# Performance work log

Measured on AMD Instinct MI355X. Metric: run time of the kernel, lower is better.

The kernel has to match this reference:

```python
import jax, jax.numpy as jnp
import numpy as np

EPS = 1e-7  # tf.keras.backend.epsilon()
ROUTING_ITERS = 3


def setup_inputs() -> dict:
    key = jax.random.key(0)
    k1, k2 = jax.random.split(key)
    B, I, Din = 64, 4096, 8
    N, D = 10, 16
    inputs = jax.random.normal(k1, (B, I, Din), dtype=jnp.float32)
    # glorot_uniform-ish init for W [I, N, Din, D]
    limit = (6.0 / (Din + D)) ** 0.5
    W = jax.random.uniform(k2, (I, N, Din, D), dtype=jnp.float32, minval=-limit, maxval=limit)
    return {"inputs": inputs, "W": W}


def _elementwise_squash(s):
    # Original squashes over axis=-2 of [B,1,N,1,D], a size-1 axis ->
    # the reduce_sum is a no-op and squash becomes elementwise.
    sq = s * s
    scale = sq / (1.0 + sq) / jnp.sqrt(sq + EPS)
    return scale * s


def reference(inputs, W):
    # inputs: [B, I, Din], W: [I, N, Din, D]
    # u_hat[b,i,n,d] = sum_p inputs[b,i,p] * W[i,n,p,d]  (the tile+matmul)
    u_hat = jnp.einsum('bip,inpd->bind', inputs, W)  # [B, I, N, D]
    B, I, N, D = u_hat.shape
    b = jnp.zeros((B, I, N, 1), dtype=u_hat.dtype)
    v = None
    for it in range(ROUTING_ITERS):
        c = jax.nn.softmax(b, axis=2)                 # [B, I, N, 1]
        s = jnp.sum(c * u_hat, axis=1)                # [B, N, D]
        v = _elementwise_squash(s)                    # [B, N, D]
        if it < ROUTING_ITERS - 1:
            # agreement: sum over D -> [B, I, N, 1]
            b = b + jnp.sum(u_hat * v[:, None, :, :], axis=-1, keepdims=True)
    # original: squeeze(v[B,1,N,1,D], axis=1) -> [B, N, 1, D]
    return v[:, :, None, :]
```

## Files before the change

kernel.cpp:

```cpp
#include <hip/hip_runtime.h>
#include <math.h>

#define B_ 64
#define I_ 4096
#define P_ 8
#define N_ 10
#define D_ 16
#define ND_ 160
#define BND_ (B_*ND_)
#define EPS_ 1e-7f

#define IPB_ 8
#define ROWS_ (I_ / IPB_)
#define WTILE_ (N_ * P_ * D_)
#define LGS_ 11

__global__ __launch_bounds__(256)
void xT_kernel(const float* __restrict__ x, float* __restrict__ xT)
{
    int idx = blockIdx.x * 256 + threadIdx.x;
    int p = idx & 7;
    int i = (idx >> 3) & (I_ - 1);
    int b = idx >> 15;
    xT[((size_t)i * B_ + b) * P_ + p] = x[idx];
}

template<int MODE>
__global__ __launch_bounds__(320)
void digitcaps_pass(const float* __restrict__ xT, const float* __restrict__ W,
                    const float* __restrict__ Vc, float* __restrict__ part)
{
    __shared__ float wsh[IPB_ * WTILE_];
    __shared__ float lgsh[(MODE == 1) ? 2 : 1][B_][LGS_];
    const int t = threadIdx.x;
    const int b = t & 63;
    const int w = t >> 6;
    const int n0 = 2 * w;
    const int i0 = blockIdx.x * IPB_;

    {
        const float4* __restrict__ Wg = (const float4*)(W + (size_t)i0 * WTILE_);
        float4* __restrict__ Ws = (float4*)wsh;
#pragma unroll
        for (int c = 0; c < (IPB_ * WTILE_) / 4 / 320; ++c)
            Ws[c * 320 + t] = Wg[c * 320 + t];
    }

    float vc[2][D_];
    if (MODE == 1) {
#pragma unroll
        for (int q = 0; q < 2; ++q) {
            const float4* vp = (const float4*)(Vc + (size_t)b * ND_ + (n0 + q) * D_);
#pragma unroll
            for (int d4 = 0; d4 < 4; ++d4) {
                float4 vv = vp[d4];
                vc[q][d4 * 4 + 0] = vv.x; vc[q][d4 * 4 + 1] = vv.y;
                vc[q][d4 * 4 + 2] = vv.z; vc[q][d4 * 4 + 3] = vv.w;
            }
        }
    }

    float acc[2][D_];
#pragma unroll
    for (int q = 0; q < 2; ++q)
#pragma unroll
        for (int d = 0; d < D_; ++d) acc[q][d] = 0.f;

    float xv[P_];
    {
        const float4* xp = (const float4*)(xT + ((size_t)i0 * B_ + b) * P_);
        float4 a0 = xp[0], a1 = xp[1];
        xv[0]=a0.x; xv[1]=a0.y; xv[2]=a0.z; xv[3]=a0.w;
        xv[4]=a1.x; xv[5]=a1.y; xv[6]=a1.z; xv[7]=a1.w;
    }

    __syncthreads();

#pragma unroll 1
    for (int il = 0; il < IPB_; ++il) {
        const float* __restrict__ Wt = wsh + il * WTILE_ + n0 * (P_ * D_);
        float tv[2][D_];
#pragma unroll
        for (int q = 0; q < 2; ++q) {
            const float* __restrict__ Wq = Wt + q * (P_ * D_);
#pragma unroll
            for (int d = 0; d < D_; ++d) tv[q][d] = 0.f;
#pragma unroll
            for (int p = 0; p < P_; ++p) {
                const float4* __restrict__ wp = (const float4*)(Wq + p * D_);
#pragma unroll
                for (int d4 = 0; d4 < 4; ++d4) {
                    float4 wv = wp[d4];
                    tv[q][d4 * 4 + 0] = fmaf(wv.x, xv[p], tv[q][d4 * 4 + 0]);
                    tv[q][d4 * 4 + 1] = fmaf(wv.y, xv[p], tv[q][d4 * 4 + 1]);
                    tv[q][d4 * 4 + 2] = fmaf(wv.z, xv[p], tv[q][d4 * 4 + 2]);
                    tv[q][d4 * 4 + 3] = fmaf(wv.w, xv[p], tv[q][d4 * 4 + 3]);
                }
            }
        }

        float xn[P_];
        if (il + 1 < IPB_) {
            const float4* xp = (const float4*)(xT + ((size_t)(i0 + il + 1) * B_ + b) * P_);
            float4 a0 = xp[0], a1 = xp[1];
            xn[0]=a0.x; xn[1]=a0.y; xn[2]=a0.z; xn[3]=a0.w;
            xn[4]=a1.x; xn[5]=a1.y; xn[6]=a1.z; xn[7]=a1.w;
        }

        if (MODE == 0) {
#pragma unroll
            for (int q = 0; q < 2; ++q)
#pragma unroll
                for (int d = 0; d < D_; ++d) acc[q][d] += tv[q][d];
        } else {
            float lgq[2];
#pragma unroll
            for (int q = 0; q < 2; ++q) {
                float lA = 0.f, lB = 0.f;
#pragma unroll
                for (int d = 0; d < 8; ++d) {
                    lA = fmaf(tv[q][d], vc[q][d], lA);
                    lB = fmaf(tv[q][d + 8], vc[q][d + 8], lB);
                }
                lgq[q] = lA + lB;
            }
            const int buf = il & 1;
            lgsh[buf][b][n0]     = lgq[0];
            lgsh[buf][b][n0 + 1] = lgq[1];
            __syncthreads();
            float lg[N_];
#pragma unroll
            for (int n = 0; n < N_; ++n) lg[n] = lgsh[buf][b][n];
            float m = lg[0];
#pragma unroll
            for (int n = 1; n < N_; ++n) m = fmaxf(m, lg[n]);
            float se = 0.f;
#pragma unroll
            for (int n = 0; n < N_; ++n) se += __expf(lg[n] - m);
            float inv = 1.f / se;
            float cq0 = __expf(lgq[0] - m) * inv;
            float cq1 = __expf(lgq[1] - m) * inv;
#pragma unroll
            for (int d = 0; d < D_; ++d) {
                acc[0][d] = fmaf(cq0, tv[0][d], acc[0][d]);
                acc[1][d] = fmaf(cq1, tv[1][d], acc[1][d]);
            }
        }

#pragma unroll
        for (int p = 0; p < P_; ++p) xv[p] = xn[p];
    }

    float* __restrict__ po = part + (size_t)blockIdx.x * BND_;
#pragma unroll
    for (int q = 0; q < 2; ++q)
#pragma unroll
        for (int d = 0; d < D_; ++d)
            po[((n0 + q) * D_ + d) * B_ + b] = acc[q][d];
}

__global__ __launch_bounds__(256)
void digitcaps_reduce(const float* __restrict__ part, int rows,
                      float scale, int mode,
                      float* __restrict__ Vc, float* __restrict__ out)
{
    __shared__ float sm[4][16];
    const int t = threadIdx.x;
    const int kk = t & 15;
    const int tp = t >> 4;
    const int k = blockIdx.x * 16 + kk;

    float s = 0.f;
    const int steps = rows >> 4;
    const float* __restrict__ p0 = part + (size_t)tp * BND_ + k;
    const size_t stride = (size_t)16 * BND_;
#pragma unroll 8
    for (int j = 0; j < steps; ++j)
        s += p0[(size_t)j * stride];

    s += __shfl_down(s, 32);
    s += __shfl_down(s, 16);
    if ((t & 63) < 16) sm[t >> 6][kk] = s;
    __syncthreads();

    if (t < 16) {
        float tot = (sm[0][t] + sm[1][t]) + (sm[2][t] + sm[3][t]);
        tot *= scale;
        float sq = tot * tot;
        float v = tot * (sq / ((1.f + sq) * sqrtf(sq + EPS_)));
        int k2 = blockIdx.x * 16 + t;
        int j = (k2 & 63) * ND_ + (k2 >> 6);
        if (mode == 0)      Vc[j] = v;
        else if (mode == 1) Vc[j] += v;
        else                out[j] = v;
    }
}

extern "C" void kernel_launch(void* const* d_in, const int* in_sizes, int n_in,
                              void* d_out, int out_size, void* d_ws, size_t ws_size,
                              hipStream_t stream)
{
    const float* x = (const float*)d_in[0];
    const float* W = (const float*)d_in[1];
    float* out = (float*)d_out;

    float* part = (float*)d_ws;
    float* Vc   = part + (size_t)ROWS_ * BND_;
    float* xT   = Vc + BND_;

    dim3 pblk(320), pgrid(ROWS_), rblk(256), rgrid(BND_ / 16);

    xT_kernel<<<dim3((B_ * I_ * P_) / 256), dim3(256), 0, stream>>>(x, xT);

    for (int pass = 0; pass < 3; ++pass) {
        if (pass == 0)
            digitcaps_pass<0><<<pgrid, pblk, 0, stream>>>(xT, W, nullptr, part);
        else
            digitcaps_pass<1><<<pgrid, pblk, 0, stream>>>(xT, W, Vc, part);
        digitcaps_reduce<<<rgrid, rblk, 0, stream>>>(part, ROWS_,
                                                     pass == 0 ? 0.1f : 1.0f, pass, Vc, out);
    }
}
```

Baseline: 186.9 us.

## Remap threads to 4 lanes per batch with DPP softmax and drop transpose

The pass kernel now gives each batch element 4 lanes (n parity × d half), so each wave covers 16 batches and a block has 256 threads. The softmax over capsules uses DPP lane exchanges instead of a shared-memory logits buffer and __syncthreads on every input row. The separate x transpose kernel is removed; x is read directly in its native layout and partials are written b-major with float4 stores. The trade-off is uncoalesced x reads (each lane group reads different batches), 4x redundant x loads per batch, and more work per thread.

```diff
diff --git a/kernel.cpp b/kernel.cpp
--- a/kernel.cpp
+++ b/kernel.cpp
@@ -11,64 +11,58 @@
 #define EPS_ 1e-7f
 
 #define IPB_ 8
-#define ROWS_ (I_ / IPB_)
+#define NBLK_ (I_ / IPB_)
 #define WTILE_ (N_ * P_ * D_)
-#define LGS_ 11
-
-__global__ __launch_bounds__(256)
-void xT_kernel(const float* __restrict__ x, float* __restrict__ xT)
-{
-    int idx = blockIdx.x * 256 + threadIdx.x;
-    int p = idx & 7;
-    int i = (idx >> 3) & (I_ - 1);
-    int b = idx >> 15;
-    xT[((size_t)i * B_ + b) * P_ + p] = x[idx];
+
+template<int CTRL>
+__device__ __forceinline__ float dpp_bcast(float v) {
+    int r = __builtin_amdgcn_update_dpp(0, __float_as_int(v), CTRL, 0xF, 0xF, true);
+    return __int_as_float(r);
 }
 
 template<int MODE>
-__global__ __launch_bounds__(320)
-void digitcaps_pass(const float* __restrict__ xT, const float* __restrict__ W,
+__global__ __launch_bounds__(256, 2)
+void digitcaps_pass(const float* __restrict__ x, const float* __restrict__ W,
                     const float* __restrict__ Vc, float* __restrict__ part)
 {
     __shared__ float wsh[IPB_ * WTILE_];
-    __shared__ float lgsh[(MODE == 1) ? 2 : 1][B_][LGS_];
     const int t = threadIdx.x;
-    const int b = t & 63;
-    const int w = t >> 6;
-    const int n0 = 2 * w;
+    const int lane = t & 63;
+    const int dh = lane & 1;
+    const int np = (lane >> 1) & 1;
+    const int bl = lane >> 2;
+    const int wv = t >> 6;
+    const int b  = wv * 16 + bl;
     const int i0 = blockIdx.x * IPB_;
 
     {
         const float4* __restrict__ Wg = (const float4*)(W + (size_t)i0 * WTILE_);
         float4* __restrict__ Ws = (float4*)wsh;
 #pragma unroll
-        for (int c = 0; c < (IPB_ * WTILE_) / 4 / 320; ++c)
-            Ws[c * 320 + t] = Wg[c * 320 + t];
-    }
-
-    float vc[2][D_];
+        for (int c = 0; c < (IPB_ * WTILE_) / (4 * 256); ++c)
+            Ws[c * 256 + t] = Wg[c * 256 + t];
+    }
+
+    float vc[5][8];
     if (MODE == 1) {
 #pragma unroll
-        for (int q = 0; q < 2; ++q) {
-            const float4* vp = (const float4*)(Vc + (size_t)b * ND_ + (n0 + q) * D_);
-#pragma unroll
-            for (int d4 = 0; d4 < 4; ++d4) {
-                float4 vv = vp[d4];
-                vc[q][d4 * 4 + 0] = vv.x; vc[q][d4 * 4 + 1] = vv.y;
-                vc[q][d4 * 4 + 2] = vv.z; vc[q][d4 * 4 + 3] = vv.w;
-            }
-        }
-    }
-
-    float acc[2][D_];
-#pragma unroll
-    for (int q = 0; q < 2; ++q)
-#pragma unroll
-        for (int d = 0; d < D_; ++d) acc[q][d] = 0.f;
+        for (int k = 0; k < 5; ++k) {
+            const float4* vp = (const float4*)(Vc + (size_t)b * ND_ + (np + 2 * k) * D_ + dh * 8);
+            float4 v0 = vp[0], v1 = vp[1];
+            vc[k][0]=v0.x; vc[k][1]=v0.y; vc[k][2]=v0.z; vc[k][3]=v0.w;
+            vc[k][4]=v1.x; vc[k][5]=v1.y; vc[k][6]=v1.z; vc[k][7]=v1.w;
+        }
+    }
+
+    float acc[5][8];
+#pragma unroll
+    for (int k = 0; k < 5; ++k)
+#pragma unroll
+        for (int d = 0; d < 8; ++d) acc[k][d] = 0.f;
 
     float xv[P_];
     {
-        const float4* xp = (const float4*)(xT + ((size_t)i0 * B_ + b) * P_);
+        const float4* xp = (const float4*)(x + ((size_t)b * I_ + i0) * P_);
         float4 a0 = xp[0], a1 = xp[1];
         xv[0]=a0.x; xv[1]=a0.y; xv[2]=a0.z; xv[3]=a0.w;
         xv[4]=a1.x; xv[5]=a1.y; xv[6]=a1.z; xv[7]=a1.w;
@@ -78,30 +72,33 @@
 
 #pragma unroll 1
     for (int il = 0; il < IPB_; ++il) {
-        const float* __restrict__ Wt = wsh + il * WTILE_ + n0 * (P_ * D_);
-        float tv[2][D_];
-#pragma unroll
-        for (int q = 0; q < 2; ++q) {
-            const float* __restrict__ Wq = Wt + q * (P_ * D_);
-#pragma unroll
-            for (int d = 0; d < D_; ++d) tv[q][d] = 0.f;
+        const float* __restrict__ Wt = wsh + il * WTILE_ + dh * 8;
+
+        float tv[5][8];
+#pragma unroll
+        for (int k = 0; k < 5; ++k) {
+            const float* __restrict__ Wn = Wt + (np + 2 * k) * (P_ * D_);
+#pragma unroll
+            for (int d = 0; d < 8; ++d) tv[k][d] = 0.f;
 #pragma unroll
             for (int p = 0; p < P_; ++p) {
-                const float4* __restrict__ wp = (const float4*)(Wq + p * D_);
-#pragma unroll
-                for (int d4 = 0; d4 < 4; ++d4) {
-                    float4 wv = wp[d4];
-                    tv[q][d4 * 4 + 0] = fmaf(wv.x, xv[p], tv[q][d4 * 4 + 0]);
-                    tv[q][d4 * 4 + 1] = fmaf(wv.y, xv[p], tv[q][d4 * 4 + 1]);
-                    tv[q][d4 * 4 + 2] = fmaf(wv.z, xv[p], tv[q][d4 * 4 + 2]);
-                    tv[q][d4 * 4 + 3] = fmaf(wv.w, xv[p], tv[q][d4 * 4 + 3]);
-                }
+                const float4* __restrict__ wp = (const float4*)(Wn + p * D_);
+                float4 wa = wp[0], wb = wp[1];
+                float xp = xv[p];
+                tv[k][0] = fmaf(wa.x, xp, tv[k][0]);
+                tv[k][1] = fmaf(wa.y, xp, tv[k][1]);
+                tv[k][2] = fmaf(wa.z, xp, tv[k][2]);
+                tv[k][3] = fmaf(wa.w, xp, tv[k][3]);
+                tv[k][4] = fmaf(wb.x, xp, tv[k][4]);
+                tv[k][5] = fmaf(wb.y, xp, tv[k][5]);
+                tv[k][6] = fmaf(wb.z, xp, tv[k][6]);
+                tv[k][7] = fmaf(wb.w, xp, tv[k][7]);
             }
         }
 
         float xn[P_];
         if (il + 1 < IPB_) {
-            const float4* xp = (const float4*)(xT + ((size_t)(i0 + il + 1) * B_ + b) * P_);
+            const float4* xp = (const float4*)(x + ((size_t)b * I_ + i0 + il + 1) * P_);
             float4 a0 = xp[0], a1 = xp[1];
             xn[0]=a0.x; xn[1]=a0.y; xn[2]=a0.z; xn[3]=a0.w;
             xn[4]=a1.x; xn[5]=a1.y; xn[6]=a1.z; xn[7]=a1.w;
@@ -109,59 +106,55 @@
 
         if (MODE == 0) {
 #pragma unroll
-            for (int q = 0; q < 2; ++q)
-#pragma unroll
-                for (int d = 0; d < D_; ++d) acc[q][d] += tv[q][d];
+            for (int k = 0; k < 5; ++k)
+#pragma unroll
+                for (int d = 0; d < 8; ++d) acc[k][d] += tv[k][d];
         } else {
-            float lgq[2];
-#pragma unroll
-            for (int q = 0; q < 2; ++q) {
-                float lA = 0.f, lB = 0.f;
-#pragma unroll
-                for (int d = 0; d < 8; ++d) {
-                    lA = fmaf(tv[q][d], vc[q][d], lA);
-                    lB = fmaf(tv[q][d + 8], vc[q][d + 8], lB);
-                }
-                lgq[q] = lA + lB;
+            float e[5];
+            float m = -1e30f;
+#pragma unroll
+            for (int k = 0; k < 5; ++k) {
+                float l = 0.f;
+#pragma unroll
+                for (int d = 0; d < 8; ++d) l = fmaf(tv[k][d], vc[k][d], l);
+                l += dpp_bcast<0xB1>(l);
+                e[k] = l;
+                m = fmaxf(m, l);
             }
-            const int buf = il & 1;
-            lgsh[buf][b][n0]     = lgq[0];
-            lgsh[buf][b][n0 + 1] = lgq[1];
-            __syncthreads();
-            float lg[N_];
-#pragma unroll
-            for (int n = 0; n < N_; ++n) lg[n] = lgsh[buf][b][n];
-            float m = lg[0];
-#pragma unroll
-            for (int n = 1; n < N_; ++n) m = fmaxf(m, lg[n]);
+            m = fmaxf(m, dpp_bcast<0x4E>(m));
             float se = 0.f;
 #pragma unroll
-            for (int n = 0; n < N_; ++n) se += __expf(lg[n] - m);
+            for (int k = 0; k < 5; ++k) { e[k] = __expf(e[k] - m); se += e[k]; }
+            se += dpp_bcast<0x4E>(se);
             float inv = 1.f / se;
-            float cq0 = __expf(lgq[0] - m) * inv;
-            float cq1 = __expf(lgq[1] - m) * inv;
-#pragma unroll
-            for (int d = 0; d < D_; ++d) {
-                acc[0][d] = fmaf(cq0, tv[0][d], acc[0][d]);
-                acc[1][d] = fmaf(cq1, tv[1][d], acc[1][d]);
+#pragma unroll
+            for (int k = 0; k < 5; ++k) {
+                float cn = e[k] * inv;
+#pragma unroll
+                for (int d = 0; d < 8; ++d)
+                    acc[k][d] = fmaf(cn, tv[k][d], acc[k][d]);
             }
         }
 
-#pragma unroll
-        for (int p = 0; p < P_; ++p) xv[p] = xn[p];
-    }
-
-    float* __restrict__ po = part + (size_t)blockIdx.x * BND_;
-#pragma unroll
-    for (int q = 0; q < 2; ++q)
-#pragma unroll
-        for (int d = 0; d < D_; ++d)
-            po[((n0 + q) * D_ + d) * B_ + b] = acc[q][d];
+        if (il + 1 < IPB_) {
+#pragma unroll
+            for (int p = 0; p < P_; ++p) xv[p] = xn[p];
+        }
+    }
+
+    float* __restrict__ po = part + (size_t)blockIdx.x * BND_ + (size_t)b * ND_;
+#pragma unroll
+    for (int k = 0; k < 5; ++k) {
+        float* dst = po + (np + 2 * k) * D_ + dh * 8;
+        float4 s0 = {acc[k][0], acc[k][1], acc[k][2], acc[k][3]};
+        float4 s1 = {acc[k][4], acc[k][5], acc[k][6], acc[k][7]};
+        *(float4*)(dst)     = s0;
+        *(float4*)(dst + 4) = s1;
+    }
 }
 
 __global__ __launch_bounds__(256)
-void digitcaps_reduce(const float* __restrict__ part, int rows,
-                      float scale, int mode,
+void digitcaps_reduce(const float* __restrict__ part, float scale, int mode,
                       float* __restrict__ Vc, float* __restrict__ out)
 {
     __shared__ float sm[4][16];
@@ -171,12 +164,10 @@
     const int k = blockIdx.x * 16 + kk;
 
     float s = 0.f;
-    const int steps = rows >> 4;
     const float* __restrict__ p0 = part + (size_t)tp * BND_ + k;
-    const size_t stride = (size_t)16 * BND_;
 #pragma unroll 8
-    for (int j = 0; j < steps; ++j)
-        s += p0[(size_t)j * stride];
+    for (int j = 0; j < NBLK_ / 16; ++j)
+        s += p0[(size_t)j * 16 * BND_];
 
     s += __shfl_down(s, 32);
     s += __shfl_down(s, 16);
@@ -188,8 +179,7 @@
         tot *= scale;
         float sq = tot * tot;
         float v = tot * (sq / ((1.f + sq) * sqrtf(sq + EPS_)));
-        int k2 = blockIdx.x * 16 + t;
-        int j = (k2 & 63) * ND_ + (k2 >> 6);
+        int j = blockIdx.x * 16 + t;
         if (mode == 0)      Vc[j] = v;
         else if (mode == 1) Vc[j] += v;
         else                out[j] = v;
@@ -205,19 +195,16 @@
     float* out = (float*)d_out;
 
     float* part = (float*)d_ws;
-    float* Vc   = part + (size_t)ROWS_ * BND_;
-    float* xT   = Vc + BND_;
-
-    dim3 pblk(320), pgrid(ROWS_), rblk(256), rgrid(BND_ / 16);
-
-    xT_kernel<<<dim3((B_ * I_ * P_) / 256), dim3(256), 0, stream>>>(x, xT);
+    float* Vc   = part + (size_t)NBLK_ * BND_;
+
+    dim3 pblk(256), pgrid(NBLK_), rblk(256), rgrid(BND_ / 16);
 
     for (int pass = 0; pass < 3; ++pass) {
         if (pass == 0)
-            digitcaps_pass<0><<<pgrid, pblk, 0, stream>>>(xT, W, nullptr, part);
+            digitcaps_pass<0><<<pgrid, pblk, 0, stream>>>(x, W, nullptr, part);
         else
-            digitcaps_pass<1><<<pgrid, pblk, 0, stream>>>(xT, W, Vc, part);
-        digitcaps_reduce<<<rgrid, rblk, 0, stream>>>(part, ROWS_,
-                                                     pass == 0 ? 0.1f : 1.0f, pass, Vc, out);
-    }
-}
+            digitcaps_pass<1><<<pgrid, pblk, 0, stream>>>(x, W, Vc, part);
+        digitcaps_reduce<<<rgrid, rblk, 0, stream>>>(part, pass == 0 ? 0.1f : 1.0f,
+                                                     pass, Vc, out);
+    }
+}
```

Measured after the change: 171.5 us. -8.3%, faster.
